# Performance work log

Measured on AMD Instinct MI355X. Metric: run time of the kernel, lower is better.

## Reference

```python
import jax, jax.numpy as jnp
import numpy as np

B, T, C, H = 8, 4096, 384, 64

def setup_inputs() -> dict:
    key = jax.random.key(0)
    k1, k2, k3, k4 = jax.random.split(key, 4)
    x = jax.random.normal(k1, (B, T, C), dtype=jnp.float32)
    # nn.Linear(C, H, bias=False) weight applied as x @ W (W stored [C, H])
    s = 1.0 / np.sqrt(C)
    Wk = jax.random.normal(k2, (C, H), dtype=jnp.float32) * s
    Wq = jax.random.normal(k3, (C, H), dtype=jnp.float32) * s
    Wv = jax.random.normal(k4, (C, H), dtype=jnp.float32) * s
    return {"x": x, "Wk": Wk, "Wq": Wq, "Wv": Wv}

def reference(x, Wk, Wq, Wv):
    Bx, Tx, Cx = x.shape
    k = x @ Wk  # [B,T,H]
    q = x @ Wq  # [B,T,H]
    v = x @ Wv  # [B,T,H]
    # NOTE: original scales by C**-0.5 (embedding dim), not head_size**-0.5
    w = jnp.einsum('bth,bsh->bts', q, k) * (Cx ** -0.5)  # [B,T,T]
    causal = jnp.tril(jnp.ones((Tx, Tx), dtype=bool))
    w = jnp.where(causal, w, -jnp.inf)
    w = jax.nn.softmax(w, axis=-1)
    # dropout omitted (eval mode / deterministic reference)
    out = jnp.einsum('bts,bsh->bth', w, v)  # [B,T,H]
    return out
```

## Files before the change

### kernel.cpp

```cpp
#include <hip/hip_runtime.h>
#include <hip/hip_bf16.h>


typedef __bf16 bf16x8 __attribute__((ext_vector_type(8)));
typedef float  f32x4  __attribute__((ext_vector_type(4)));

#define BB   8
#define TT   4096
#define CC   384
#define HH   64
#define NROW (BB*TT)
#define QSCALE (0.05103103630798288f * 1.4426950408889634f)

#if __has_builtin(__builtin_amdgcn_exp2f)
#define EXP2(x) __builtin_amdgcn_exp2f(x)
#else
#define EXP2(x) exp2f(x)
#endif

__device__ __forceinline__ unsigned short f2bf(float f) {
    __bf16 h = (__bf16)f;
    return __builtin_bit_cast(unsigned short, h);
}

__global__ __launch_bounds__(256) void wtrans_kernel(
        const float* __restrict__ Wk,
        const float* __restrict__ Wq,
        const float* __restrict__ Wv,
        unsigned short* __restrict__ Wt) {
    __shared__ __align__(16) unsigned short tile[64][72];
    const float* Wm = (blockIdx.y == 0) ? Wk : ((blockIdx.y == 1) ? Wq : Wv);
    unsigned short* Wtm = Wt + blockIdx.y * (HH * CC);
    const int c0 = blockIdx.x * 64;
#pragma unroll
    for (int i = 0; i < 16; ++i) {
        int id = threadIdx.x + i * 256;
        int c = id >> 6, h = id & 63;
        tile[c][h] = f2bf(Wm[(c0 + c) * HH + h]);
    }
    __syncthreads();
#pragma unroll
    for (int i = 0; i < 16; ++i) {
        int id = threadIdx.x + i * 256;
        int h = id >> 6, c = id & 63;
        Wtm[h * CC + c0 + c] = tile[c][h];
    }
}

__global__ __launch_bounds__(512, 4) void qkv_kernel(
        const float* __restrict__ x,
        const unsigned short* __restrict__ Wt,
        unsigned short* __restrict__ q_ws,
        unsigned short* __restrict__ k_ws,
        unsigned short* __restrict__ vt_ws) {
    __shared__ __align__(16) f32x4 xacc[256 * 13];
    __shared__ __align__(16) unsigned short vtile[64][72];

    const int lane = threadIdx.x & 63;
    const int wv8  = threadIdx.x >> 6;
    const int grp  = wv8 >> 2;
    const int wg   = wv8 & 3;
    const int g256 = threadIdx.x & 255;
    const int l15  = lane & 15;
    const int quad = lane >> 4;
    const int rb   = blockIdx.x * 64;
    const int row  = rb + wg * 16 + l15;

    const float* xbase = x + (long)row * CC + grp * 192 + quad * 8;
    float4 xr[12];
#pragma unroll
    for (int i = 0; i < 6; ++i) {
        xr[2 * i]     = *reinterpret_cast<const float4*>(xbase + i * 32);
        xr[2 * i + 1] = *reinterpret_cast<const float4*>(xbase + i * 32 + 4);
    }
    bf16x8 a[6];
#pragma unroll
    for (int i = 0; i < 6; ++i) {
        a[i][0] = (__bf16)xr[2 * i].x;     a[i][1] = (__bf16)xr[2 * i].y;
        a[i][2] = (__bf16)xr[2 * i].z;     a[i][3] = (__bf16)xr[2 * i].w;
        a[i][4] = (__bf16)xr[2 * i + 1].x; a[i][5] = (__bf16)xr[2 * i + 1].y;
        a[i][6] = (__bf16)xr[2 * i + 1].z; a[i][7] = (__bf16)xr[2 * i + 1].w;
    }

    f32x4 acc[3][4];
    const f32x4 zero = {0.f, 0.f, 0.f, 0.f};
#pragma unroll
    for (int m = 0; m < 3; ++m)
#pragma unroll
        for (int nt = 0; nt < 4; ++nt) acc[m][nt] = zero;

#pragma unroll
    for (int i = 0; i < 6; ++i) {
        const int gcoff = grp * 192 + i * 32 + quad * 8;
#pragma unroll
        for (int m = 0; m < 3; ++m) {
            const unsigned short* wtm = Wt + m * (HH * CC);
#pragma unroll
            for (int nt = 0; nt < 4; ++nt) {
                bf16x8 bfr = *reinterpret_cast<const bf16x8*>(
                    wtm + (nt * 16 + l15) * CC + gcoff);
                acc[m][nt] = __builtin_amdgcn_mfma_f32_16x16x32_bf16(
                    a[i], bfr, acc[m][nt], 0, 0, 0);
            }
        }
    }

    const int cidx = g256 * 13;
    if (grp == 1) {
#pragma unroll
        for (int m = 0; m < 3; ++m)
#pragma unroll
            for (int nt = 0; nt < 4; ++nt)
                xacc[cidx + m * 4 + nt] = acc[m][nt];
    }
    __syncthreads();

    if (grp == 0) {
#pragma unroll
        for (int m = 0; m < 3; ++m)
#pragma unroll
            for (int nt = 0; nt < 4; ++nt)
                acc[m][nt] += xacc[cidx + m * 4 + nt];

#pragma unroll
        for (int nt = 0; nt < 4; ++nt) {
            const int h  = nt * 16 + l15;
            const int c8 = h >> 3;
            const int jj = h & 7;
#pragma unroll
            for (int r = 0; r < 4; ++r) {
                const int gr = rb + wg * 16 + quad * 4 + r;
                const int ii = quad * 4 + r;
                const int s   = gr & 63;
                const int stp = ((s >> 4) & 2) + ((s >> 2) & 1);
                const int ip  = ((s >> 1) & 12) + (s & 3);
                k_ws[(long)(gr >> 6) * 4096 + stp * 1024 + c8 * 128 + ip * 8 + jj]
                    = f2bf(acc[0][nt][r]);
                q_ws[gr * HH + h] = f2bf(acc[1][nt][r] * QSCALE);
                vtile[h][ii + wg * 16] = f2bf(acc[2][nt][r]);
            }
        }
    }
    __syncthreads();
    {
        int id = threadIdx.x;
        int dt = id >> 7, sc = (id >> 4) & 7, ii = id & 15;
        unsigned short* dst = vt_ws + (long)(rb >> 6) * 4096
                              + (dt * 8 + sc) * 128 + ii * 8;
        *reinterpret_cast<uint4*>(dst) =
            *reinterpret_cast<const uint4*>(&vtile[dt * 16 + ii][sc * 8]);
    }
}

__global__ __launch_bounds__(1024, 4) void attn_kernel(
        const unsigned short* __restrict__ q_ws,
        const unsigned short* __restrict__ k_ws,
        const unsigned short* __restrict__ vt_ws,
        float* __restrict__ out) {
    __shared__ __align__(16) float xchg[64 * 65];
    __shared__ float mx1[64], lx1[64];

    const int lane = threadIdx.x & 63;
    const int wv16 = threadIdx.x >> 6;
    const int grp  = wv16 >> 2;
    const int wg   = wv16 & 3;
    const int l15  = lane & 15;
    const int quad = lane >> 4;

    const int bid = blockIdx.x;
    const int b   = bid & 7;
    const int p   = bid >> 3;

    const f32x4 zero = {0.f, 0.f, 0.f, 0.f};

    auto do_tile = [&](int t, int qt, int qrow,
                       const bf16x8& qf0, const bf16x8& qf1,
                       f32x4* o, float& mprev, float& lsum) {
        const int s0 = t * 64;
        const unsigned short* ktile = k_ws + ((long)((b * TT + s0) >> 4)) * 1024;
        const unsigned short* vtile = vt_ws + ((long)((b * TT + s0) >> 6)) * 4096;

        bf16x8 ka0[4], ka1[4];
#pragma unroll
        for (int st = 0; st < 4; ++st) {
            ka0[st] = *reinterpret_cast<const bf16x8*>(
                ktile + ((st * 8 + quad) * 16 + l15) * 8);
            ka1[st] = *reinterpret_cast<const bf16x8*>(
                ktile + ((st * 8 + 4 + quad) * 16 + l15) * 8);
        }
        bf16x8 vb0[4], vb1[4];
#pragma unroll
        for (int dt = 0; dt < 4; ++dt) {
            vb0[dt] = *reinterpret_cast<const bf16x8*>(
                vtile + dt * 1024 + quad * 128 + l15 * 8);
            vb1[dt] = *reinterpret_cast<const bf16x8*>(
                vtile + dt * 1024 + (4 + quad) * 128 + l15 * 8);
        }

        f32x4 sc[4];
#pragma unroll
        for (int st = 0; st < 4; ++st) {
            f32x4 z = zero;
            z = __builtin_amdgcn_mfma_f32_16x16x32_bf16(ka0[st], qf0, z, 0, 0, 0);
            z = __builtin_amdgcn_mfma_f32_16x16x32_bf16(ka1[st], qf1, z, 0, 0, 0);
            sc[st] = z;
        }

        if (t == qt) {
#pragma unroll
            for (int st = 0; st < 4; ++st)
#pragma unroll
                for (int r = 0; r < 4; ++r) {
                    int sg = s0 + ((st >> 1) << 5) + (quad << 3)
                               + ((st & 1) << 2) + r;
                    if (sg > qrow) sc[st][r] = -1e30f;
                }
        }

        float mloc = -1e30f;
#pragma unroll
        for (int st = 0; st < 4; ++st)
#pragma unroll
            for (int r = 0; r < 4; ++r) mloc = fmaxf(mloc, sc[st][r]);
        mloc = fmaxf(mloc, __shfl_xor(mloc, 16));
        mloc = fmaxf(mloc, __shfl_xor(mloc, 32));
        const float mnew = fmaxf(mprev, mloc);
        const unsigned long long anych = __ballot(mnew > mprev);
        float alpha = 1.0f;
        if (anych) alpha = EXP2(mprev - mnew);

        float psum = 0.f;
#pragma unroll
        for (int st = 0; st < 4; ++st)
#pragma unroll
            for (int r = 0; r < 4; ++r) {
                float pv = EXP2(sc[st][r] - mnew);
                psum += pv;
                sc[st][r] = pv;
            }
        psum += __shfl_xor(psum, 16);
        psum += __shfl_xor(psum, 32);
        lsum = lsum * alpha + psum;
        mprev = mnew;

        if (anych) {
            float ar[4];
#pragma unroll
            for (int r = 0; r < 4; ++r) ar[r] = __shfl(alpha, quad * 4 + r);
#pragma unroll
            for (int dt = 0; dt < 4; ++dt)
#pragma unroll
                for (int r = 0; r < 4; ++r) o[dt][r] *= ar[r];
        }

        bf16x8 pf0, pf1;
#pragma unroll
        for (int r = 0; r < 4; ++r) {
            pf0[r]     = (__bf16)sc[0][r];
            pf0[4 + r] = (__bf16)sc[1][r];
            pf1[r]     = (__bf16)sc[2][r];
            pf1[4 + r] = (__bf16)sc[3][r];
        }
#pragma unroll
        for (int dt = 0; dt < 4; ++dt) {
            o[dt] = __builtin_amdgcn_mfma_f32_16x16x32_bf16(pf0, vb0[dt], o[dt], 0, 0, 0);
            o[dt] = __builtin_amdgcn_mfma_f32_16x16x32_bf16(pf1, vb1[dt], o[dt], 0, 0, 0);
        }
    };

    auto merge_store = [&](int qt, f32x4* o, float& mprev, float& lsum) {
        for (int rr = 1; rr < 4; ++rr) {
            __syncthreads();
            if (grp == rr) {
                if (quad == 0) { mx1[wg * 16 + l15] = mprev; lx1[wg * 16 + l15] = lsum; }
#pragma unroll
                for (int dt = 0; dt < 4; ++dt)
#pragma unroll
                    for (int r = 0; r < 4; ++r)
                        xchg[(wg * 16 + quad * 4 + r) * 65 + dt * 16 + l15] = o[dt][r];
            }
            __syncthreads();
            if (grp == 0) {
#pragma unroll
                for (int r = 0; r < 4; ++r) {
                    const int row = wg * 16 + quad * 4 + r;
                    const float m0r = __shfl(mprev, quad * 4 + r);
                    const float m1r = mx1[row];
                    const float ms  = fmaxf(m0r, m1r);
                    const float w0  = EXP2(m0r - ms);
                    const float w1  = EXP2(m1r - ms);
#pragma unroll
                    for (int dt = 0; dt < 4; ++dt)
                        o[dt][r] = o[dt][r] * w0 + xchg[row * 65 + dt * 16 + l15] * w1;
                }
                const float m1l = mx1[wg * 16 + l15];
                const float msl = fmaxf(mprev, m1l);
                lsum = EXP2(mprev - msl) * lsum + EXP2(m1l - msl) * lx1[wg * 16 + l15];
                mprev = msl;
            }
        }
        if (grp == 0) {
            float rl[4];
#pragma unroll
            for (int r = 0; r < 4; ++r) rl[r] = 1.0f / __shfl(lsum, quad * 4 + r);
            const int orow = qt * 64 + wg * 16 + quad * 4;
#pragma unroll
            for (int dt = 0; dt < 4; ++dt)
#pragma unroll
                for (int r = 0; r < 4; ++r)
                    out[(long)(b * TT + orow + r) * HH + dt * 16 + l15] = o[dt][r] * rl[r];
        }
        __syncthreads();
    };

    {
        const int qt = 63 - p;
        const int qrow = qt * 64 + wg * 16 + l15;
        const unsigned short* qbase = q_ws + (b * TT + qrow) * HH;
        const bf16x8 qf0 = *reinterpret_cast<const bf16x8*>(qbase + quad * 8);
        const bf16x8 qf1 = *reinterpret_cast<const bf16x8*>(qbase + 32 + quad * 8);
        f32x4 o[4];
#pragma unroll
        for (int dt = 0; dt < 4; ++dt) o[dt] = zero;
        float mprev = -1e30f, lsum = 0.f;
        for (int t = grp; t <= qt; t += 4)
            do_tile(t, qt, qrow, qf0, qf1, o, mprev, lsum);
        merge_store(qt, o, mprev, lsum);
    }

    {
        const int qt = p;
        const int qrow = qt * 64 + wg * 16 + l15;
        const unsigned short* qbase = q_ws + (b * TT + qrow) * HH;
        const bf16x8 qf0 = *reinterpret_cast<const bf16x8*>(qbase + quad * 8);
        const bf16x8 qf1 = *reinterpret_cast<const bf16x8*>(qbase + 32 + quad * 8);
        f32x4 o[4];
#pragma unroll
        for (int dt = 0; dt < 4; ++dt) o[dt] = zero;
        float mprev = -1e30f, lsum = 0.f;
        for (int t = grp; t <= qt; t += 4)
            do_tile(t, qt, qrow, qf0, qf1, o, mprev, lsum);
        merge_store(qt, o, mprev, lsum);
    }
}

extern "C" void kernel_launch(void* const* d_in, const int* in_sizes, int n_in,
                              void* d_out, int out_size, void* d_ws, size_t ws_size,
                              hipStream_t stream) {
    const float* x  = (const float*)d_in[0];
    const float* Wk = (const float*)d_in[1];
    const float* Wq = (const float*)d_in[2];
    const float* Wv = (const float*)d_in[3];
    float* out = (float*)d_out;

    char* ws = (char*)d_ws;
    unsigned short* Wt    = (unsigned short*)(ws);
    unsigned short* q_ws  = (unsigned short*)(ws + 147456);
    unsigned short* k_ws  = (unsigned short*)(ws + 147456 + 4194304);
    unsigned short* vt_ws = (unsigned short*)(ws + 147456 + 2 * 4194304);

    wtrans_kernel<<<dim3(6, 3), 256, 0, stream>>>(Wk, Wq, Wv, Wt);
    qkv_kernel<<<NROW / 64, 512, 0, stream>>>(x, Wt, q_ws, k_ws, vt_ws);
    attn_kernel<<<(TT / 128) * BB, 1024, 0, stream>>>(q_ws, k_ws, vt_ws, out);
}
```

Baseline: 164.1 us.

## Restructure QKV projection with double-buffered async global-to-LDS x staging

The QKV projection kernel now handles 32 rows per 256-thread block instead of 64 rows per 512 threads, and drops the cross-group split-K reduction through shared memory. Activations are streamed in 64-column chunks straight into a double-buffered, XOR-swizzled LDS tile using global_load_lds, so the next chunk's load overlaps the MFMAs on the current one. Each wave computes a 16-row by 32-column slice of all three projections. The goal is to hide global load latency and cut register pressure. In exchange it adds a barrier per chunk, and the attention kernel dominates total time anyway.

```diff
diff --git a/kernel.cpp b/kernel.cpp
--- a/kernel.cpp
+++ b/kernel.cpp
@@ -47,108 +47,115 @@
     }
 }
 
-__global__ __launch_bounds__(512, 4) void qkv_kernel(
+__global__ __launch_bounds__(256, 4) void qkv_kernel(
         const float* __restrict__ x,
         const unsigned short* __restrict__ Wt,
         unsigned short* __restrict__ q_ws,
         unsigned short* __restrict__ k_ws,
         unsigned short* __restrict__ vt_ws) {
-    __shared__ __align__(16) f32x4 xacc[256 * 13];
-    __shared__ __align__(16) unsigned short vtile[64][72];
+    __shared__ __align__(16) float xs[2][32][64];
+    __shared__ __align__(16) unsigned short vtile[64][40];
 
     const int lane = threadIdx.x & 63;
-    const int wv8  = threadIdx.x >> 6;
-    const int grp  = wv8 >> 2;
-    const int wg   = wv8 & 3;
-    const int g256 = threadIdx.x & 255;
+    const int wv   = threadIdx.x >> 6;
+    const int rt   = wv & 1;
+    const int hh   = wv >> 1;
     const int l15  = lane & 15;
     const int quad = lane >> 4;
-    const int rb   = blockIdx.x * 64;
-    const int row  = rb + wg * 16 + l15;
-
-    const float* xbase = x + (long)row * CC + grp * 192 + quad * 8;
-    float4 xr[12];
-#pragma unroll
-    for (int i = 0; i < 6; ++i) {
-        xr[2 * i]     = *reinterpret_cast<const float4*>(xbase + i * 32);
-        xr[2 * i + 1] = *reinterpret_cast<const float4*>(xbase + i * 32 + 4);
-    }
-    bf16x8 a[6];
-#pragma unroll
-    for (int i = 0; i < 6; ++i) {
-        a[i][0] = (__bf16)xr[2 * i].x;     a[i][1] = (__bf16)xr[2 * i].y;
-        a[i][2] = (__bf16)xr[2 * i].z;     a[i][3] = (__bf16)xr[2 * i].w;
-        a[i][4] = (__bf16)xr[2 * i + 1].x; a[i][5] = (__bf16)xr[2 * i + 1].y;
-        a[i][6] = (__bf16)xr[2 * i + 1].z; a[i][7] = (__bf16)xr[2 * i + 1].w;
-    }
-
-    f32x4 acc[3][4];
+    const int rb   = blockIdx.x * 32;
+
+    auto stage = [&](int kk, int bb) {
+#pragma unroll
+        for (int j = 0; j < 2; ++j) {
+            const int r0 = wv * 8 + j * 4;
+            const int r  = r0 + quad;
+            const int ch = l15 ^ (r & 7);
+            const float* src = x + (long)(rb + r) * CC + kk * 64 + ch * 4;
+            float* dst = &xs[bb][r0][0];
+            __builtin_amdgcn_global_load_lds(
+                (const __attribute__((address_space(1))) unsigned int*)src,
+                (__attribute__((address_space(3))) unsigned int*)dst,
+                16, 0, 0);
+        }
+    };
+
+    f32x4 acc[3][2];
     const f32x4 zero = {0.f, 0.f, 0.f, 0.f};
 #pragma unroll
     for (int m = 0; m < 3; ++m)
 #pragma unroll
-        for (int nt = 0; nt < 4; ++nt) acc[m][nt] = zero;
-
-#pragma unroll
-    for (int i = 0; i < 6; ++i) {
-        const int gcoff = grp * 192 + i * 32 + quad * 8;
-#pragma unroll
-        for (int m = 0; m < 3; ++m) {
-            const unsigned short* wtm = Wt + m * (HH * CC);
-#pragma unroll
-            for (int nt = 0; nt < 4; ++nt) {
-                bf16x8 bfr = *reinterpret_cast<const bf16x8*>(
-                    wtm + (nt * 16 + l15) * CC + gcoff);
-                acc[m][nt] = __builtin_amdgcn_mfma_f32_16x16x32_bf16(
-                    a[i], bfr, acc[m][nt], 0, 0, 0);
-            }
-        }
-    }
-
-    const int cidx = g256 * 13;
-    if (grp == 1) {
-#pragma unroll
-        for (int m = 0; m < 3; ++m)
-#pragma unroll
-            for (int nt = 0; nt < 4; ++nt)
-                xacc[cidx + m * 4 + nt] = acc[m][nt];
-    }
+        for (int n = 0; n < 2; ++n) acc[m][n] = zero;
+
+    const int ntb = hh * 2;
+    const int rloc = rt * 16 + l15;
+    const int rx7  = rloc & 7;
+
+    stage(0, 0);
+    __asm volatile("s_waitcnt vmcnt(0)" ::: "memory");
     __syncthreads();
 
-    if (grp == 0) {
-#pragma unroll
-        for (int m = 0; m < 3; ++m)
-#pragma unroll
-            for (int nt = 0; nt < 4; ++nt)
-                acc[m][nt] += xacc[cidx + m * 4 + nt];
-
-#pragma unroll
-        for (int nt = 0; nt < 4; ++nt) {
-            const int h  = nt * 16 + l15;
-            const int c8 = h >> 3;
-            const int jj = h & 7;
-#pragma unroll
-            for (int r = 0; r < 4; ++r) {
-                const int gr = rb + wg * 16 + quad * 4 + r;
-                const int ii = quad * 4 + r;
-                const int s   = gr & 63;
-                const int stp = ((s >> 4) & 2) + ((s >> 2) & 1);
-                const int ip  = ((s >> 1) & 12) + (s & 3);
-                k_ws[(long)(gr >> 6) * 4096 + stp * 1024 + c8 * 128 + ip * 8 + jj]
-                    = f2bf(acc[0][nt][r]);
-                q_ws[gr * HH + h] = f2bf(acc[1][nt][r] * QSCALE);
-                vtile[h][ii + wg * 16] = f2bf(acc[2][nt][r]);
-            }
+    int cur = 0;
+#pragma unroll
+    for (int kk = 0; kk < 6; ++kk) {
+        if (kk < 5) stage(kk + 1, cur ^ 1);
+#pragma unroll
+        for (int h01 = 0; h01 < 2; ++h01) {
+            const int chb = 8 * h01 + 2 * quad;
+            const f32x4 xa = *reinterpret_cast<const f32x4*>(
+                &xs[cur][rloc][((chb) ^ rx7) * 4]);
+            const f32x4 xb = *reinterpret_cast<const f32x4*>(
+                &xs[cur][rloc][((chb + 1) ^ rx7) * 4]);
+            bf16x8 a;
+#pragma unroll
+            for (int e = 0; e < 4; ++e) {
+                a[e]     = (__bf16)xa[e];
+                a[4 + e] = (__bf16)xb[e];
+            }
+            const int gcoff = kk * 64 + h01 * 32 + quad * 8;
+#pragma unroll
+            for (int m = 0; m < 3; ++m) {
+                const unsigned short* wtm = Wt + m * (HH * CC);
+#pragma unroll
+                for (int n = 0; n < 2; ++n) {
+                    bf16x8 bfr = *reinterpret_cast<const bf16x8*>(
+                        wtm + ((ntb + n) * 16 + l15) * CC + gcoff);
+                    acc[m][n] = __builtin_amdgcn_mfma_f32_16x16x32_bf16(
+                        a, bfr, acc[m][n], 0, 0, 0);
+                }
+            }
+        }
+        __asm volatile("s_waitcnt vmcnt(0)" ::: "memory");
+        __syncthreads();
+        cur ^= 1;
+    }
+
+#pragma unroll
+    for (int n = 0; n < 2; ++n) {
+        const int nt = ntb + n;
+        const int h  = nt * 16 + l15;
+        const int c8 = h >> 3;
+        const int jj = h & 7;
+#pragma unroll
+        for (int r = 0; r < 4; ++r) {
+            const int gr = rb + rt * 16 + quad * 4 + r;
+            const int s   = gr & 63;
+            const int stp = ((s >> 4) & 2) + ((s >> 2) & 1);
+            const int ip  = ((s >> 1) & 12) + (s & 3);
+            k_ws[(long)(gr >> 6) * 4096 + stp * 1024 + c8 * 128 + ip * 8 + jj]
+                = f2bf(acc[0][n][r]);
+            q_ws[gr * HH + h] = f2bf(acc[1][n][r] * QSCALE);
+            vtile[h][rt * 16 + quad * 4 + r] = f2bf(acc[2][n][r]);
         }
     }
     __syncthreads();
     {
-        int id = threadIdx.x;
-        int dt = id >> 7, sc = (id >> 4) & 7, ii = id & 15;
+        const int id  = threadIdx.x;
+        const int dt  = id >> 6, scl = (id >> 4) & 3, ii = id & 15;
+        const int sc  = scl + ((rb >> 3) & 4);
         unsigned short* dst = vt_ws + (long)(rb >> 6) * 4096
                               + (dt * 8 + sc) * 128 + ii * 8;
         *reinterpret_cast<uint4*>(dst) =
-            *reinterpret_cast<const uint4*>(&vtile[dt * 16 + ii][sc * 8]);
+            *reinterpret_cast<const uint4*>(&vtile[dt * 16 + ii][scl * 8]);
     }
 }
 
@@ -360,6 +367,6 @@
     unsigned short* vt_ws = (unsigned short*)(ws + 147456 + 2 * 4194304);
 
     wtrans_kernel<<<dim3(6, 3), 256, 0, stream>>>(Wk, Wq, Wv, Wt);
-    qkv_kernel<<<NROW / 64, 512, 0, stream>>>(x, Wt, q_ws, k_ws, vt_ws);
+    qkv_kernel<<<NROW / 32, 256, 0, stream>>>(x, Wt, q_ws, k_ws, vt_ws);
     attn_kernel<<<(TT / 128) * BB, 1024, 0, stream>>>(q_ws, k_ws, vt_ws, out);
 }
```

Measured after the change: 161.8 us. No clear change (-1.4%).
